# Optimization experiments

Measured on AMD Instinct MI355X. Metric: run time of the kernel, lower is better.

Reference implementation:

```python
import jax, jax.numpy as jnp
import numpy as np

D_MODEL = 1024
N_HEADS = 16
D_K = D_MODEL // N_HEADS
B, S = 4, 2048


def setup_inputs() -> dict:
    key = jax.random.key(0)
    ks = jax.random.split(key, 12)
    scale = 1.0 / np.sqrt(D_MODEL)
    mk = lambda k: (jax.random.uniform(k, (D_MODEL, D_MODEL), jnp.float32, -scale, scale))
    mb = lambda k: (jax.random.uniform(k, (D_MODEL,), jnp.float32, -scale, scale))
    mask = jnp.tril(jnp.ones((S, S), dtype=bool))[None, None, :, :]  # [1,1,S,S] causal
    return {
        "query": jax.random.normal(ks[0], (B, S, D_MODEL), jnp.float32),
        "key": jax.random.normal(ks[1], (B, S, D_MODEL), jnp.float32),
        "value": jax.random.normal(ks[2], (B, S, D_MODEL), jnp.float32),
        "w_q": mk(ks[3]), "b_q": mb(ks[4]),
        "w_k": mk(ks[5]), "b_k": mb(ks[6]),
        "w_v": mk(ks[7]), "b_v": mb(ks[8]),
        "w_o": mk(ks[9]), "b_o": mb(ks[10]),
        "mask": mask,
    }


def _split_heads(x):
    b, s, _ = x.shape
    return x.reshape(b, s, N_HEADS, D_K).transpose(0, 2, 1, 3)  # [B,H,S,Dk]


def reference(query, key, value, w_q, b_q, w_k, b_k, w_v, b_v, w_o, b_o, mask):
    Q = _split_heads(query @ w_q.T + b_q)
    K = _split_heads(key @ w_k.T + b_k)
    V = _split_heads(value @ w_v.T + b_v)
    scores = jnp.einsum("bhqd,bhkd->bhqk", Q, K) / jnp.sqrt(jnp.asarray(D_K, Q.dtype))
    min_val = jnp.finfo(scores.dtype).min
    scores = jnp.where(mask, scores, min_val)
    attn = jax.nn.softmax(scores, axis=-1)
    ctx = jnp.einsum("bhqk,bhkd->bhqd", attn, V)
    ctx = ctx.transpose(0, 2, 1, 3).reshape(query.shape[0], -1, D_MODEL)
    return ctx @ w_o.T + b_o
```

## Files before the change

### kernel.cpp

```cpp
#include <hip/hip_runtime.h>
#include <cstdint>
#include <cstddef>

#define DM 1024
#define NH 16
#define DK 64
#define BB 4
#define SS 2048
#define MROWS (BB*SS)

#define NE_ ((size_t)MROWS * DM)
#define WE_ ((size_t)DM * DM)

typedef __attribute__((ext_vector_type(8))) __bf16 bf16x8;
typedef __attribute__((ext_vector_type(4))) float f32x4;
typedef __attribute__((ext_vector_type(8))) unsigned short ushort8;

#define SCALE_LOG2E 0.18033688011112042f

__device__ __forceinline__ unsigned short f2bf(float f) {
  union { float f; unsigned u; } v; v.f = f;
  unsigned r = v.u + 0x7fffu + ((v.u >> 16) & 1u);
  return (unsigned short)(r >> 16);
}

__device__ __forceinline__ unsigned short f2bf_hw(float f) {
  __bf16 h = (__bf16)f;
  return __builtin_bit_cast(unsigned short, h);
}

__device__ __forceinline__ void async_load16(const void* g, void* l) {
  __builtin_amdgcn_global_load_lds(
      (__attribute__((address_space(1))) void*)(g),
      (__attribute__((address_space(3))) void*)(l),
      16, 0, 0);
}

template<int CTRL>
__device__ __forceinline__ float dppf(float v) {
  int i = __builtin_bit_cast(int, v);
  int r = __builtin_amdgcn_update_dpp(i, i, CTRL, 0xf, 0xf, true);
  return __builtin_bit_cast(float, r);
}
__device__ __forceinline__ float redsum16(float v) {
  v += dppf<0x128>(v);
  v += dppf<0x124>(v);
  v += dppf<0x122>(v);
  v += dppf<0x121>(v);
  return v;
}

struct CvtArgs {
  const float* src[4];
  unsigned short* dst[4];
};

__global__ __launch_bounds__(256)
void cvt_all(CvtArgs a) {
  size_t i = ((size_t)blockIdx.x * 256 + threadIdx.x) * 4;
  int seg = (int)(i >> 20);
  size_t off = i & (WE_ - 1);
  float4 v = *reinterpret_cast<const float4*>(a.src[seg] + off);
  ushort4 o;
  o.x = f2bf(v.x); o.y = f2bf(v.y); o.z = f2bf(v.z); o.w = f2bf(v.w);
  *reinterpret_cast<ushort4*>(a.dst[seg] + off) = o;
}

struct QkvArgs {
  const float* A[3];
  const unsigned short* W[3];
  const float* bias[3];
  unsigned short* out[3];
};

#define GLOAD(B, K0, RL) { \
    _Pragma("unroll") \
    for (int p_ = 0; p_ < 2; ++p_) { \
      int idx_ = (p_ * 256 + tid) * 8; \
      int row_ = idx_ >> 5; \
      int sc_  = ((tid & 3) ^ ((row_ >> 1) & 3)) * 8; \
      const float* ap_ = &A[(size_t)(gm0 + row_) * DM + (K0) + sc_]; \
      RL[p_][0] = *reinterpret_cast<const float4*>(ap_); \
      RL[p_][1] = *reinterpret_cast<const float4*>(ap_ + 4); \
      async_load16(&Bw[(size_t)(gn0 + row_) * DM + (K0) + sc_], &Bs[B][idx_]); \
    } }

#define GWRITE(B, RW) { \
    _Pragma("unroll") \
    for (int p_ = 0; p_ < 2; ++p_) { \
      int idx_ = (p_ * 256 + tid) * 8; \
      ushort8 w_; \
      _Pragma("unroll") \
      for (int j_ = 0; j_ < 4; ++j_) { \
        w_[j_]     = f2bf_hw(RW[p_][0][j_]); \
        w_[4 + j_] = f2bf_hw(RW[p_][1][j_]); \
      } \
      *reinterpret_cast<ushort8*>(&As[B][idx_]) = w_; \
    } }

#define GCOMPUTE(BUFA, BUFB) { \
    bf16x8 af[4], bfr[4]; \
    _Pragma("unroll") \
    for (int m_ = 0; m_ < 4; ++m_) { \
      int row_ = wm*64 + m_*16 + lrow; \
      af[m_] = *reinterpret_cast<const bf16x8*>(&As[BUFA][row_*32 + ((kg ^ ((row_>>1)&3)))*8]); \
    } \
    _Pragma("unroll") \
    for (int n_ = 0; n_ < 4; ++n_) { \
      int row_ = wn*64 + n_*16 + lrow; \
      bfr[n_] = *reinterpret_cast<const bf16x8*>(&Bs[BUFB][row_*32 + ((kg ^ ((row_>>1)&3)))*8]); \
    } \
    __builtin_amdgcn_s_setprio(1); \
    _Pragma("unroll") \
    for (int m_ = 0; m_ < 4; ++m_) \
      _Pragma("unroll") \
      for (int n_ = 0; n_ < 4; ++n_) \
        acc[m_][n_] = __builtin_amdgcn_mfma_f32_16x16x32_bf16(af[m_], bfr[n_], acc[m_][n_], 0, 0, 0); \
    __builtin_amdgcn_s_setprio(0); \
  }

#define GITER(KT, RL, RW) { \
    if ((KT) + 2 < 32) { GLOAD(((KT) + 2) % 3, ((KT) + 2) * 32, RL); } \
    if ((KT) + 1 < 32) { \
      if ((KT) + 2 < 32) { asm volatile("s_waitcnt vmcnt(6)" ::: "memory"); } \
      else               { asm volatile("s_waitcnt vmcnt(0)" ::: "memory"); } \
      GWRITE(((KT) + 1) & 1, RW); \
    } \
    GCOMPUTE((KT) & 1, (KT) % 3); \
    asm volatile("s_waitcnt lgkmcnt(0)" ::: "memory"); \
    __builtin_amdgcn_s_barrier(); \
    __builtin_amdgcn_sched_barrier(0); \
  }

#define GKLOOP_F32A() { \
    float4 ra0[2][2], ra1[2][2]; \
    GLOAD(0, 0, ra0); \
    GLOAD(1, 32, ra1); \
    asm volatile("s_waitcnt vmcnt(6)" ::: "memory"); \
    GWRITE(0, ra0); \
    asm volatile("s_waitcnt lgkmcnt(0)" ::: "memory"); \
    __builtin_amdgcn_s_barrier(); \
    __builtin_amdgcn_sched_barrier(0); \
    for (int kt = 0; kt < 32; kt += 2) { \
      GITER(kt,     ra0, ra1); \
      GITER(kt + 1, ra1, ra0); \
    } \
  }

__global__ __launch_bounds__(256)
void gemm_qkv(QkvArgs qa)
{
  __shared__ __align__(16) unsigned short As[2][128*32];
  __shared__ __align__(16) unsigned short Bs[3][128*32];

  int wgid = blockIdx.x + blockIdx.y * 24;
  wgid = (wgid & 7) * 192 + (wgid >> 3);
  const int bx = wgid % 24, by = wgid / 24;

  const int sel = bx >> 3;
  const float* __restrict__ A = qa.A[sel];
  const unsigned short* __restrict__ Bw = qa.W[sel];
  const float* __restrict__ bias = qa.bias[sel];
  unsigned short* __restrict__ o = qa.out[sel];
  const float qs = (sel == 0) ? SCALE_LOG2E : 1.0f;

  const int tid  = threadIdx.x;
  const int lane = tid & 63;
  const int wv   = tid >> 6;
  const int wm   = wv >> 1, wn = wv & 1;
  const int gm0  = by * 128;
  const int gn0  = (bx & 7) * 128;
  const int lrow = lane & 15;
  const int kg   = lane >> 4;

  f32x4 acc[4][4] = {};

  GKLOOP_F32A();

  const int orow = (lane >> 4) * 4;
  const int ocol = lane & 15;
  if (sel != 2) {
    #pragma unroll
    for (int n = 0; n < 4; ++n) {
      int gn = gn0 + wn*64 + n*16 + ocol;
      float bv = bias[gn] * qs;
      int h = gn >> 6, d = gn & (DK - 1);
      #pragma unroll
      for (int m = 0; m < 4; ++m) {
        #pragma unroll
        for (int r = 0; r < 4; ++r) {
          int gm = gm0 + wm*64 + m*16 + orow + r;
          int b = gm >> 11, s = gm & (SS - 1);
          o[(((size_t)b*NH + h)*SS + s)*DK + d] = f2bf_hw(fmaf(acc[m][n][r], qs, bv));
        }
      }
    }
  } else {
    #pragma unroll
    for (int n = 0; n < 4; ++n) {
      int gn = gn0 + wn*64 + n*16 + ocol;
      float bv = bias[gn];
      int h = gn >> 6, d = gn & (DK - 1);
      #pragma unroll
      for (int m = 0; m < 4; ++m) {
        int s0 = gm0 + wm*64 + m*16 + orow;
        int b  = s0 >> 11, s = s0 & (SS - 1);
        ushort4 w;
        w.x = f2bf_hw(acc[m][n][0] + bv);
        w.y = f2bf_hw(acc[m][n][1] + bv);
        w.z = f2bf_hw(acc[m][n][2] + bv);
        w.w = f2bf_hw(acc[m][n][3] + bv);
        *reinterpret_cast<ushort4*>(&o[(((size_t)b*NH + h)*DK + d)*SS + s]) = w;
      }
    }
  }
}

#define GSTAGE(B, K0) { \
    _Pragma("unroll") \
    for (int p_ = 0; p_ < 2; ++p_) { \
      int idx_ = (p_ * 256 + tid) * 8; \
      int row_ = idx_ >> 5; \
      int sc_  = ((tid & 3) ^ ((row_ >> 1) & 3)) * 8; \
      async_load16(&A [(size_t)(gm0 + row_) * DM + (K0) + sc_], &As[B][idx_]); \
      async_load16(&Bw[(size_t)(gn0 + row_) * DM + (K0) + sc_], &Bs[B][idx_]); \
    } }

__global__ __launch_bounds__(256)
void gemm_out(const unsigned short* __restrict__ A,
              const unsigned short* __restrict__ Bw,
              const float* __restrict__ bias,
              float* __restrict__ o)
{
  __shared__ __align__(16) unsigned short As[3][128*32];
  __shared__ __align__(16) unsigned short Bs[3][128*32];

  int wgid = blockIdx.x + blockIdx.y * 8;
  wgid = (wgid & 7) * 64 + (wgid >> 3);
  const int bx = wgid & 7, by = wgid >> 3;

  const int tid  = threadIdx.x;
  const int lane = tid & 63;
  const int wv   = tid >> 6;
  const int wm   = wv >> 1, wn = wv & 1;
  const int gm0  = by * 128;
  const int gn0  = bx * 128;
  const int lrow = lane & 15;
  const int kg   = lane >> 4;

  f32x4 acc[4][4] = {};

  GSTAGE(0, 0);
  GSTAGE(1, 32);
  for (int kt = 0; kt < 31; ++kt) {
    asm volatile("s_waitcnt vmcnt(4)" ::: "memory");
    __builtin_amdgcn_s_barrier();
    __builtin_amdgcn_sched_barrier(0);
    if (kt + 2 < 32) { GSTAGE((kt + 2) % 3, (kt + 2) * 32); }
    GCOMPUTE(kt % 3, kt % 3);
  }
  asm volatile("s_waitcnt vmcnt(0)" ::: "memory");
  __builtin_amdgcn_s_barrier();
  __builtin_amdgcn_sched_barrier(0);
  GCOMPUTE(1, 1);

  const int orow = (lane >> 4) * 4;
  const int ocol = lane & 15;
  #pragma unroll
  for (int n = 0; n < 4; ++n) {
    int gn = gn0 + wn*64 + n*16 + ocol;
    float bv = bias[gn];
    #pragma unroll
    for (int m = 0; m < 4; ++m)
      #pragma unroll
      for (int r = 0; r < 4; ++r) {
        int gm = gm0 + wm*64 + m*16 + orow + r;
        o[(size_t)gm * DM + gn] = acc[m][n][r] + bv;
      }
  }
}

__global__ __launch_bounds__(512)
void attn_kernel(const unsigned short* __restrict__ Qp,
                 const unsigned short* __restrict__ Kp,
                 const unsigned short* __restrict__ VpT,
                 unsigned short* __restrict__ ctx)
{
  __shared__ __align__(16) unsigned short Kb[2][64*64];
  __shared__ __align__(16) unsigned short Vb[2][64*64];
  __shared__ __align__(16) unsigned short Ps[8][16][72];

  const int tid  = threadIdx.x;
  const int lane = tid & 63;
  const int w    = tid >> 6;
  const int bh   = blockIdx.x;
  const int qt   = gridDim.y - 1 - blockIdx.y;
  const int qb0  = qt * 128;
  const int qw0  = qb0 + w * 16;
  const int lrow = lane & 15;
  const int g0   = lane >> 4;
  const int lk8  = g0 * 8;

  const size_t qbase = ((size_t)bh * SS + qw0 + lrow) * DK;
  bf16x8 aq0 = *reinterpret_cast<const bf16x8*>(&Qp[qbase + lk8]);
  bf16x8 aq1 = *reinterpret_cast<const bf16x8*>(&Qp[qbase + 32 + lk8]);

  f32x4 accc[4] = {};
  float psum[4] = {0.f, 0.f, 0.f, 0.f};

  const int ntiles = 2*qt + 2;
  const int twlast = (qw0 + 15) >> 6;
  const int srow   = tid >> 3;
  const int ssrc   = (tid & 7) ^ (srow & 7);

#define STAGE(B, T) { \
    const int kv0_ = (T) * 64; \
    async_load16(&Kp [((size_t)bh*SS + kv0_ + srow)*DK + ssrc*8], &Kb[B][tid*8]); \
    async_load16(&VpT[((size_t)bh*DK + srow)*SS + kv0_ + ssrc*8], &Vb[B][tid*8]); }

  STAGE(0, 0);

  for (int t = 0; t < ntiles; ++t) {
    const int buf = t & 1;
    asm volatile("s_waitcnt vmcnt(0)" ::: "memory");
    __syncthreads();
    if (t + 1 < ntiles) { if (buf) { STAGE(0, t + 1); } else { STAGE(1, t + 1); } }

    if (t <= twlast) {
      const int kv0 = t * 64;
      const unsigned short* Kc = &Kb[buf][0];
      const unsigned short* Vc = &Vb[buf][0];

      f32x4 sc[4];
      __builtin_amdgcn_s_setprio(1);
      #pragma unroll
      for (int kb = 0; kb < 4; ++kb) {
        const int rk = kb*16 + lrow;
        const int cx = rk & 7;
        bf16x8 bk0 = *reinterpret_cast<const bf16x8*>(&Kc[rk*64 + ((g0    ) ^ cx)*8]);
        bf16x8 bk1 = *reinterpret_cast<const bf16x8*>(&Kc[rk*64 + ((g0 + 4) ^ cx)*8]);
        f32x4 z = {};
        z      = __builtin_amdgcn_mfma_f32_16x16x32_bf16(aq0, bk0, z, 0, 0, 0);
        sc[kb] = __builtin_amdgcn_mfma_f32_16x16x32_bf16(aq1, bk1, z, 0, 0, 0);
      }
      __builtin_amdgcn_s_setprio(0);

      const int qrow0 = qw0 + g0 * 4;
      const bool needmask = (kv0 + 63 > qw0);
      #pragma unroll
      for (int kb = 0; kb < 4; ++kb) {
        const int kvg = kv0 + kb*16 + lrow;
        #pragma unroll
        for (int r = 0; r < 4; ++r) {
          float p = __builtin_amdgcn_exp2f(sc[kb][r]);
          if (needmask && (kvg > qrow0 + r)) p = 0.f;
          sc[kb][r] = p;
          psum[r] += p;
        }
      }

      #pragma unroll
      for (int kb = 0; kb < 4; ++kb)
        #pragma unroll
        for (int r = 0; r < 4; ++r)
          Ps[w][g0*4 + r][kb*16 + lrow] = f2bf_hw(sc[kb][r]);
      asm volatile("s_waitcnt lgkmcnt(0)" ::: "memory");

      bf16x8 pa0 = *reinterpret_cast<const bf16x8*>(&Ps[w][lrow][lk8]);
      bf16x8 pa1 = *reinterpret_cast<const bf16x8*>(&Ps[w][lrow][32 + lk8]);
      __builtin_amdgcn_s_setprio(1);
      #pragma unroll
      for (int db = 0; db < 4; ++db) {
        const int rv = db*16 + lrow;
        const int cv = rv & 7;
        bf16x8 bv0 = *reinterpret_cast<const bf16x8*>(&Vc[rv*64 + ((g0    ) ^ cv)*8]);
        bf16x8 bv1 = *reinterpret_cast<const bf16x8*>(&Vc[rv*64 + ((g0 + 4) ^ cv)*8]);
        accc[db] = __builtin_amdgcn_mfma_f32_16x16x32_bf16(pa0, bv0, accc[db], 0, 0, 0);
        accc[db] = __builtin_amdgcn_mfma_f32_16x16x32_bf16(pa1, bv1, accc[db], 0, 0, 0);
      }
      __builtin_amdgcn_s_setprio(0);
    }
  }

  const int b = bh >> 4, hh = bh & (NH - 1);
  #pragma unroll
  for (int r = 0; r < 4; ++r) {
    int q = qw0 + g0*4 + r;
    float l = redsum16(psum[r]);
    float inv = __builtin_amdgcn_rcpf(l);
    size_t base = ((size_t)b * SS + q) * DM + hh * DK;
    #pragma unroll
    for (int db = 0; db < 4; ++db)
      ctx[base + db*16 + lrow] = f2bf_hw(accc[db][r] * inv);
  }
}

extern "C" void kernel_launch(void* const* d_in, const int* in_sizes, int n_in,
                              void* d_out, int out_size, void* d_ws, size_t ws_size,
                              hipStream_t stream)
{
  const float* q_in = (const float*)d_in[0];
  const float* k_in = (const float*)d_in[1];
  const float* v_in = (const float*)d_in[2];
  const float* w_q  = (const float*)d_in[3];
  const float* b_q  = (const float*)d_in[4];
  const float* w_k  = (const float*)d_in[5];
  const float* b_k  = (const float*)d_in[6];
  const float* w_v  = (const float*)d_in[7];
  const float* b_v  = (const float*)d_in[8];
  const float* w_o  = (const float*)d_in[9];
  const float* b_o  = (const float*)d_in[10];

  char* ws = (char*)d_ws;
  size_t off = 0;
  unsigned short* wb[4];
  for (int i = 0; i < 4; ++i) { wb[i] = (unsigned short*)(ws + off); off += WE_ * 2; }
  unsigned short* Qp  = (unsigned short*)(ws + off); off += NE_ * 2;
  unsigned short* Kp  = (unsigned short*)(ws + off); off += NE_ * 2;
  unsigned short* VpT = (unsigned short*)(ws + off); off += NE_ * 2;
  unsigned short* ctx = (unsigned short*)(ws + off); off += NE_ * 2;

  CvtArgs ca;
  ca.src[0] = w_q; ca.dst[0] = wb[0];
  ca.src[1] = w_k; ca.dst[1] = wb[1];
  ca.src[2] = w_v; ca.dst[2] = wb[2];
  ca.src[3] = w_o; ca.dst[3] = wb[3];
  cvt_all<<<(int)(4*WE_/1024), 256, 0, stream>>>(ca);

  QkvArgs qa;
  qa.A[0] = q_in; qa.W[0] = wb[0]; qa.bias[0] = b_q; qa.out[0] = Qp;
  qa.A[1] = k_in; qa.W[1] = wb[1]; qa.bias[1] = b_k; qa.out[1] = Kp;
  qa.A[2] = v_in; qa.W[2] = wb[2]; qa.bias[2] = b_v; qa.out[2] = VpT;
  gemm_qkv<<<dim3(24, MROWS/128), 256, 0, stream>>>(qa);

  attn_kernel<<<dim3(BB*NH, SS/128), 512, 0, stream>>>(Qp, Kp, VpT, ctx);

  gemm_out<<<dim3(DM/128, MROWS/128), 256, 0, stream>>>(ctx, wb[3], b_o, (float*)d_out);
}
```

Before: 175.3 us.

## Enlarge QKV and output GEMM tiles to 256x128 with 512-thread blocks

```diff
diff --git a/kernel.cpp b/kernel.cpp
--- a/kernel.cpp
+++ b/kernel.cpp
@@ -66,6 +66,28 @@
   *reinterpret_cast<ushort4*>(a.dst[seg] + off) = o;
 }
 
+
+#define GCOMPUTE(BUFA, BUFB) { \
+    bf16x8 af[4], bfr[4]; \
+    _Pragma("unroll") \
+    for (int m_ = 0; m_ < 4; ++m_) { \
+      int row_ = wm*64 + m_*16 + lrow; \
+      af[m_] = *reinterpret_cast<const bf16x8*>(&As[BUFA][row_*32 + ((kg ^ ((row_>>1)&3)))*8]); \
+    } \
+    _Pragma("unroll") \
+    for (int n_ = 0; n_ < 4; ++n_) { \
+      int row_ = wn*64 + n_*16 + lrow; \
+      bfr[n_] = *reinterpret_cast<const bf16x8*>(&Bs[BUFB][row_*32 + ((kg ^ ((row_>>1)&3)))*8]); \
+    } \
+    __builtin_amdgcn_s_setprio(1); \
+    _Pragma("unroll") \
+    for (int m_ = 0; m_ < 4; ++m_) \
+      _Pragma("unroll") \
+      for (int n_ = 0; n_ < 4; ++n_) \
+        acc[m_][n_] = __builtin_amdgcn_mfma_f32_16x16x32_bf16(af[m_], bfr[n_], acc[m_][n_], 0, 0, 0); \
+    __builtin_amdgcn_s_setprio(0); \
+  }
+
 struct QkvArgs {
   const float* A[3];
   const unsigned short* W[3];
@@ -73,22 +95,24 @@
   unsigned short* out[3];
 };
 
-#define GLOAD(B, K0, RL) { \
+#define QLOAD(B, K0, RL) { \
     _Pragma("unroll") \
     for (int p_ = 0; p_ < 2; ++p_) { \
-      int idx_ = (p_ * 256 + tid) * 8; \
+      int idx_ = (p_ * 512 + tid) * 8; \
       int row_ = idx_ >> 5; \
       int sc_  = ((tid & 3) ^ ((row_ >> 1) & 3)) * 8; \
       const float* ap_ = &A[(size_t)(gm0 + row_) * DM + (K0) + sc_]; \
       RL[p_][0] = *reinterpret_cast<const float4*>(ap_); \
       RL[p_][1] = *reinterpret_cast<const float4*>(ap_ + 4); \
-      async_load16(&Bw[(size_t)(gn0 + row_) * DM + (K0) + sc_], &Bs[B][idx_]); \
-    } }
-
-#define GWRITE(B, RW) { \
+    } \
+    { int brow_ = tid >> 2; \
+      int bsc_  = ((tid & 3) ^ ((brow_ >> 1) & 3)) * 8; \
+      async_load16(&Bw[(size_t)(gn0 + brow_) * DM + (K0) + bsc_], &Bs[B][tid*8]); } }
+
+#define QWRITE(B, RW) { \
     _Pragma("unroll") \
     for (int p_ = 0; p_ < 2; ++p_) { \
-      int idx_ = (p_ * 256 + tid) * 8; \
+      int idx_ = (p_ * 512 + tid) * 8; \
       ushort8 w_; \
       _Pragma("unroll") \
       for (int j_ = 0; j_ < 4; ++j_) { \
@@ -98,33 +122,12 @@
       *reinterpret_cast<ushort8*>(&As[B][idx_]) = w_; \
     } }
 
-#define GCOMPUTE(BUFA, BUFB) { \
-    bf16x8 af[4], bfr[4]; \
-    _Pragma("unroll") \
-    for (int m_ = 0; m_ < 4; ++m_) { \
-      int row_ = wm*64 + m_*16 + lrow; \
-      af[m_] = *reinterpret_cast<const bf16x8*>(&As[BUFA][row_*32 + ((kg ^ ((row_>>1)&3)))*8]); \
-    } \
-    _Pragma("unroll") \
-    for (int n_ = 0; n_ < 4; ++n_) { \
-      int row_ = wn*64 + n_*16 + lrow; \
-      bfr[n_] = *reinterpret_cast<const bf16x8*>(&Bs[BUFB][row_*32 + ((kg ^ ((row_>>1)&3)))*8]); \
-    } \
-    __builtin_amdgcn_s_setprio(1); \
-    _Pragma("unroll") \
-    for (int m_ = 0; m_ < 4; ++m_) \
-      _Pragma("unroll") \
-      for (int n_ = 0; n_ < 4; ++n_) \
-        acc[m_][n_] = __builtin_amdgcn_mfma_f32_16x16x32_bf16(af[m_], bfr[n_], acc[m_][n_], 0, 0, 0); \
-    __builtin_amdgcn_s_setprio(0); \
-  }
-
-#define GITER(KT, RL, RW) { \
-    if ((KT) + 2 < 32) { GLOAD(((KT) + 2) % 3, ((KT) + 2) * 32, RL); } \
+#define QITER(KT, RL, RW) { \
+    if ((KT) + 2 < 32) { QLOAD(((KT) + 2) % 3, ((KT) + 2) * 32, RL); } \
     if ((KT) + 1 < 32) { \
-      if ((KT) + 2 < 32) { asm volatile("s_waitcnt vmcnt(6)" ::: "memory"); } \
+      if ((KT) + 2 < 32) { asm volatile("s_waitcnt vmcnt(5)" ::: "memory"); } \
       else               { asm volatile("s_waitcnt vmcnt(0)" ::: "memory"); } \
-      GWRITE(((KT) + 1) & 1, RW); \
+      QWRITE(((KT) + 1) & 1, RW); \
     } \
     GCOMPUTE((KT) & 1, (KT) % 3); \
     asm volatile("s_waitcnt lgkmcnt(0)" ::: "memory"); \
@@ -132,29 +135,14 @@
     __builtin_amdgcn_sched_barrier(0); \
   }
 
-#define GKLOOP_F32A() { \
-    float4 ra0[2][2], ra1[2][2]; \
-    GLOAD(0, 0, ra0); \
-    GLOAD(1, 32, ra1); \
-    asm volatile("s_waitcnt vmcnt(6)" ::: "memory"); \
-    GWRITE(0, ra0); \
-    asm volatile("s_waitcnt lgkmcnt(0)" ::: "memory"); \
-    __builtin_amdgcn_s_barrier(); \
-    __builtin_amdgcn_sched_barrier(0); \
-    for (int kt = 0; kt < 32; kt += 2) { \
-      GITER(kt,     ra0, ra1); \
-      GITER(kt + 1, ra1, ra0); \
-    } \
-  }
-
-__global__ __launch_bounds__(256)
+__global__ __launch_bounds__(512)
 void gemm_qkv(QkvArgs qa)
 {
-  __shared__ __align__(16) unsigned short As[2][128*32];
+  __shared__ __align__(16) unsigned short As[2][256*32];
   __shared__ __align__(16) unsigned short Bs[3][128*32];
 
   int wgid = blockIdx.x + blockIdx.y * 24;
-  wgid = (wgid & 7) * 192 + (wgid >> 3);
+  wgid = (wgid & 7) * 96 + (wgid >> 3);
   const int bx = wgid % 24, by = wgid / 24;
 
   const int sel = bx >> 3;
@@ -167,15 +155,29 @@
   const int tid  = threadIdx.x;
   const int lane = tid & 63;
   const int wv   = tid >> 6;
-  const int wm   = wv >> 1, wn = wv & 1;
-  const int gm0  = by * 128;
+  const int wm   = wv >> 1;
+  const int wn   = wv & 1;
+  const int gm0  = by * 256;
   const int gn0  = (bx & 7) * 128;
   const int lrow = lane & 15;
   const int kg   = lane >> 4;
 
   f32x4 acc[4][4] = {};
 
-  GKLOOP_F32A();
+  {
+    float4 ra0[2][2], ra1[2][2];
+    QLOAD(0, 0, ra0);
+    QLOAD(1, 32, ra1);
+    asm volatile("s_waitcnt vmcnt(5)" ::: "memory");
+    QWRITE(0, ra0);
+    asm volatile("s_waitcnt lgkmcnt(0)" ::: "memory");
+    __builtin_amdgcn_s_barrier();
+    __builtin_amdgcn_sched_barrier(0);
+    for (int kt = 0; kt < 32; kt += 2) {
+      QITER(kt,     ra0, ra1);
+      QITER(kt + 1, ra1, ra0);
+    }
+  }
 
   const int orow = (lane >> 4) * 4;
   const int ocol = lane & 15;
@@ -216,47 +218,50 @@
   }
 }
 
-#define GSTAGE(B, K0) { \
+#define OSTAGE(B, K0) { \
     _Pragma("unroll") \
     for (int p_ = 0; p_ < 2; ++p_) { \
-      int idx_ = (p_ * 256 + tid) * 8; \
+      int idx_ = (p_ * 512 + tid) * 8; \
       int row_ = idx_ >> 5; \
       int sc_  = ((tid & 3) ^ ((row_ >> 1) & 3)) * 8; \
-      async_load16(&A [(size_t)(gm0 + row_) * DM + (K0) + sc_], &As[B][idx_]); \
-      async_load16(&Bw[(size_t)(gn0 + row_) * DM + (K0) + sc_], &Bs[B][idx_]); \
-    } }
-
-__global__ __launch_bounds__(256)
+      async_load16(&A[(size_t)(gm0 + row_) * DM + (K0) + sc_], &As[B][idx_]); \
+    } \
+    { int brow_ = tid >> 2; \
+      int bsc_  = ((tid & 3) ^ ((brow_ >> 1) & 3)) * 8; \
+      async_load16(&Bw[(size_t)(gn0 + brow_) * DM + (K0) + bsc_], &Bs[B][tid*8]); } }
+
+__global__ __launch_bounds__(512)
 void gemm_out(const unsigned short* __restrict__ A,
               const unsigned short* __restrict__ Bw,
               const float* __restrict__ bias,
               float* __restrict__ o)
 {
-  __shared__ __align__(16) unsigned short As[3][128*32];
+  __shared__ __align__(16) unsigned short As[3][256*32];
   __shared__ __align__(16) unsigned short Bs[3][128*32];
 
   int wgid = blockIdx.x + blockIdx.y * 8;
-  wgid = (wgid & 7) * 64 + (wgid >> 3);
+  wgid = (wgid & 7) * 32 + (wgid >> 3);
   const int bx = wgid & 7, by = wgid >> 3;
 
   const int tid  = threadIdx.x;
   const int lane = tid & 63;
   const int wv   = tid >> 6;
-  const int wm   = wv >> 1, wn = wv & 1;
-  const int gm0  = by * 128;
+  const int wm   = wv >> 1;
+  const int wn   = wv & 1;
+  const int gm0  = by * 256;
   const int gn0  = bx * 128;
   const int lrow = lane & 15;
   const int kg   = lane >> 4;
 
   f32x4 acc[4][4] = {};
 
-  GSTAGE(0, 0);
-  GSTAGE(1, 32);
+  OSTAGE(0, 0);
+  OSTAGE(1, 32);
   for (int kt = 0; kt < 31; ++kt) {
-    asm volatile("s_waitcnt vmcnt(4)" ::: "memory");
+    asm volatile("s_waitcnt vmcnt(3)" ::: "memory");
     __builtin_amdgcn_s_barrier();
     __builtin_amdgcn_sched_barrier(0);
-    if (kt + 2 < 32) { GSTAGE((kt + 2) % 3, (kt + 2) * 32); }
+    if (kt + 2 < 32) { OSTAGE((kt + 2) % 3, (kt + 2) * 32); }
     GCOMPUTE(kt % 3, kt % 3);
   }
   asm volatile("s_waitcnt vmcnt(0)" ::: "memory");
@@ -431,9 +436,9 @@
   qa.A[0] = q_in; qa.W[0] = wb[0]; qa.bias[0] = b_q; qa.out[0] = Qp;
   qa.A[1] = k_in; qa.W[1] = wb[1]; qa.bias[1] = b_k; qa.out[1] = Kp;
   qa.A[2] = v_in; qa.W[2] = wb[2]; qa.bias[2] = b_v; qa.out[2] = VpT;
-  gemm_qkv<<<dim3(24, MROWS/128), 256, 0, stream>>>(qa);
+  gemm_qkv<<<dim3(24, MROWS/256), 512, 0, stream>>>(qa);
 
   attn_kernel<<<dim3(BB*NH, SS/128), 512, 0, stream>>>(Qp, Kp, VpT, ctx);
 
-  gemm_out<<<dim3(DM/128, MROWS/128), 256, 0, stream>>>(ctx, wb[3], b_o, (float*)d_out);
-}
+  gemm_out<<<dim3(DM/128, MROWS/256), 512, 0, stream>>>(ctx, wb[3], b_o, (float*)d_out);
+}
```

New measurement: 196.7 us. 1.12x slower.
